# Optimization experiments

Hardware: AMD Instinct MI355X
Metric: run time of the kernel (lower is better)

Reference implementation:

```python
import jax, jax.numpy as jnp
import numpy as np

D = 300      # d_model / entity_embed_size, hard-coded in the module
TOPK = 20    # k in torch.topk


def setup_inputs() -> dict:
    key = jax.random.key(0)
    ks = jax.random.split(key, 6)
    N, T = 2, 4096
    scale = 1.0 / np.sqrt(D).astype(np.float32)
    return {
        "querys": jax.random.normal(ks[0], (N, T, D), jnp.float32),
        "keys":   jax.random.normal(ks[1], (N, T, D), jnp.float32),
        "values": jax.random.normal(ks[2], (N, T, D), jnp.float32),
        "Wq": jax.random.normal(ks[3], (D, D), jnp.float32) * scale,
        "Wk": jax.random.normal(ks[4], (D, D), jnp.float32) * scale,
        "Wv": jax.random.normal(ks[5], (D, D), jnp.float32) * scale,
        "num_heads": 6,
    }


def reference(querys, keys, values, Wq, Wk, Wv, num_heads):
    N, Tq, d = querys.shape
    h = int(num_heads)
    dh = d // h  # head dim (must divide; 300/6 = 50)

    # nn.Linear(bias=False): y = x @ W^T
    Q = querys @ Wq.T
    K = keys @ Wk.T
    V = values @ Wv.T  # computed but unused by the 'selected' attention, kept for fidelity

    # torch.cat(torch.split(X, dh, dim=2), dim=0): head index becomes major batch dim
    def to_heads(X):
        n, t, _ = X.shape
        return X.reshape(n, t, h, dh).transpose(2, 0, 1, 3).reshape(h * n, t, dh)

    Q_, K_ = to_heads(Q), to_heads(K)

    # scaled_dot_selected_product_attention
    scores = jnp.einsum('bqd,bkd->bqk', Q_, K_) / (dh ** 0.5)  # [hN, Tq, Tk]
    max_att = scores.max(axis=1)                                # [hN, Tk] (max over queries)
    top_vals, top_ids = jax.lax.top_k(max_att, TOPK)            # [hN, 20]
    probs = jax.nn.softmax(top_vals, axis=-1)                   # [hN, 20]
    # gather from K (not V!), matching the original code
    sel = jnp.take_along_axis(K_, top_ids[:, :, None], axis=1)  # [hN, 20, dh]
    out = jnp.sum(sel * probs[:, :, None], axis=1, keepdims=True)  # [hN, 1, dh]

    # torch.cat(torch.split(outputs, N, dim=0), dim=2): merge heads back on feature dim
    out = out.reshape(h, N, 1, dh).transpose(1, 2, 0, 3).reshape(N, 1, d)
    return out
```

## Files before the change

### kernel.cpp

```cpp
#include <hip/hip_runtime.h>
#include <hip/hip_bf16.h>
#include <math.h>

#define T      4096
#define Dm     300
#define NH     6
#define DH     50
#define NB     2
#define NBATCH 12
#define KTOP   20
#define NCAND  48
#define QC     4
#define RQC    16
#define NBINS  4096
#define BMAX   1024
#define WCH    30720
#define INITN  (NBATCH * T + NBATCH * NCAND + NBATCH)

typedef short  bs8  __attribute__((ext_vector_type(8)));
typedef float  f4   __attribute__((ext_vector_type(4)));

static __device__ __forceinline__ unsigned short f2bf(float f) {
    union { float f; unsigned u; } x{f};
    unsigned r = x.u + 0x7fffu + ((x.u >> 16) & 1u);
    return (unsigned short)(r >> 16);
}
static __device__ __forceinline__ float bf2f(unsigned short h) {
    union { unsigned u; float f; } x;
    x.u = ((unsigned)h) << 16;
    return x.f;
}
static __device__ __forceinline__ unsigned fkey(float f) {
    unsigned u = __float_as_uint(f);
    return (u & 0x80000000u) ? ~u : (u | 0x80000000u);
}
static __device__ __forceinline__ float fkey_inv(unsigned u) {
    return (u & 0x80000000u) ? __uint_as_float(u & 0x7fffffffu)
                             : __uint_as_float(~u);
}

__global__ __launch_bounds__(256) void wfrag_kernel(
    const float* __restrict__ Wq, const float* __restrict__ Wk,
    unsigned short* __restrict__ Whf, unsigned short* __restrict__ Wlf,
    unsigned* __restrict__ initp)
{
    for (unsigned g = blockIdx.x * 256 + threadIdx.x; g < INITN; g += gridDim.x * 256)
        initp[g] = 0u;

    const int idx = blockIdx.x * 256 + threadIdx.x;
    if (idx >= WCH) return;
    const int lane = idx & 63, rest = idx >> 6;
    const int ks = rest % 10, r2 = rest / 10;
    const int nt = r2 & 1, r3 = r2 >> 1;
    const int jtg = r3 % 12, z = r3 / 12;
    const int n16 = lane & 15, quad = lane >> 4;
    const int j = jtg * 32 + nt * 16 + n16;
    const int head = j >> 6, dd = j & 63;
    const float* W = z ? Wk : Wq;

    bs8 vh, vl;
#pragma unroll
    for (int e = 0; e < 8; ++e) {
        int k = ks * 32 + quad * 8 + e;
        float v = (dd < DH && k < 300) ? W[(head * DH + dd) * 300 + (k < 300 ? k : 0)] : 0.f;
        unsigned short h = f2bf(v);
        vh[e] = (short)h;
        vl[e] = (short)f2bf(v - bf2f(h));
    }
    *(bs8*)(Whf + (size_t)idx * 8) = vh;
    *(bs8*)(Wlf + (size_t)idx * 8) = vl;
}

__global__ __launch_bounds__(256, 1) void proj_mfma_kernel(
    const float* __restrict__ Xq, const float* __restrict__ Xk,
    const unsigned short* __restrict__ Whf, const unsigned short* __restrict__ Wlf,
    float* __restrict__ Qt, float* __restrict__ Kt,
    unsigned short* __restrict__ Qb, unsigned short* __restrict__ Kb)
{
    __shared__ unsigned short Bsh[2][2560 * 8];
    __shared__ unsigned short Tr[4][32][40];

    const int z  = blockIdx.z;
    const int jg = blockIdx.y;
    const int m0 = blockIdx.x * 128;
    const float* X = z ? Xk : Xq;
    float*          Ytf = z ? Kt : Qt;
    unsigned short* Ytb = z ? Kb : Qb;

    const int tid = threadIdx.x;
    const int wave = tid >> 6, lane = tid & 63;
    const int m16 = lane & 15, quad = lane >> 4;
    const int n = m0 >> 12, t0 = m0 & (T - 1);

    bs8 Ah[2][10], Al[2][10];
#pragma unroll
    for (int mt = 0; mt < 2; ++mt) {
        const float* rowp = X + (size_t)(m0 + wave * 32 + mt * 16 + m16) * 300;
#pragma unroll
        for (int ks = 0; ks < 10; ++ks) {
            float f[8];
            if (ks < 9) {
                float4 a = *(const float4*)(rowp + ks * 32 + quad * 8);
                float4 c = *(const float4*)(rowp + ks * 32 + quad * 8 + 4);
                f[0] = a.x; f[1] = a.y; f[2] = a.z; f[3] = a.w;
                f[4] = c.x; f[5] = c.y; f[6] = c.z; f[7] = c.w;
            } else {
#pragma unroll
                for (int e = 0; e < 8; ++e) {
                    int k = 288 + quad * 8 + e;
                    f[e] = (k < 300) ? rowp[k < 300 ? k : 0] : 0.f;
                }
            }
#pragma unroll
            for (int e = 0; e < 8; ++e) {
                unsigned short h = f2bf(f[e]);
                Ah[mt][ks][e] = (short)h;
                Al[mt][ks][e] = (short)f2bf(f[e] - bf2f(h));
            }
        }
    }

    bs8 rh[5], rl[5];
    {
        size_t cb = (size_t)(z * 12 + jg * 6) * 1280;
#pragma unroll
        for (int i = 0; i < 5; ++i) {
            int c = i * 256 + tid;
            rh[i] = *(const bs8*)(Whf + (cb + c) * 8);
            rl[i] = *(const bs8*)(Wlf + (cb + c) * 8);
        }
#pragma unroll
        for (int i = 0; i < 5; ++i) {
            int c = i * 256 + tid;
            *(bs8*)&Bsh[0][c * 8]          = rh[i];
            *(bs8*)&Bsh[0][(1280 + c) * 8] = rl[i];
        }
    }

    f4 acc[2][2] = {{{0.f,0.f,0.f,0.f},{0.f,0.f,0.f,0.f}},
                    {{0.f,0.f,0.f,0.f},{0.f,0.f,0.f,0.f}}};

    for (int jt = 0; jt < 6; ++jt) {
        __syncthreads();

        if (jt < 5) {
            size_t cb = (size_t)(z * 12 + jg * 6 + jt + 1) * 1280;
#pragma unroll
            for (int i = 0; i < 5; ++i) {
                int c = i * 256 + tid;
                rh[i] = *(const bs8*)(Whf + (cb + c) * 8);
                rl[i] = *(const bs8*)(Wlf + (cb + c) * 8);
            }
        }

        const unsigned short* Bbuf = Bsh[jt & 1];
#pragma unroll
        for (int ks = 0; ks < 10; ++ks) {
#pragma unroll
            for (int nt = 0; nt < 2; ++nt) {
                bs8 bh = *(const bs8*)&Bbuf[((nt * 10 + ks) * 64 + lane) * 8];
                bs8 bl = *(const bs8*)&Bbuf[((1280 + (nt * 10 + ks) * 64) + lane) * 8];
#pragma unroll
                for (int mt = 0; mt < 2; ++mt) {
                    acc[mt][nt] = __builtin_amdgcn_mfma_f32_16x16x32_bf16(Ah[mt][ks], bh, acc[mt][nt], 0, 0, 0);
                    acc[mt][nt] = __builtin_amdgcn_mfma_f32_16x16x32_bf16(Al[mt][ks], bh, acc[mt][nt], 0, 0, 0);
                    acc[mt][nt] = __builtin_amdgcn_mfma_f32_16x16x32_bf16(Ah[mt][ks], bl, acc[mt][nt], 0, 0, 0);
                }
            }
        }

        const int jtg  = jg * 6 + jt;
        const int head = jtg >> 1, d0 = (jtg & 1) * 32;
        const int b    = head * NB + n;

#pragma unroll
        for (int nt = 0; nt < 2; ++nt) {
            const int dd = d0 + nt * 16 + m16;
            if (dd < DH) {
                float* base = Ytf + ((size_t)b * DH + dd) * T + t0 + wave * 32;
#pragma unroll
                for (int mt = 0; mt < 2; ++mt)
                    *(float4*)(base + mt * 16 + quad * 4) =
                        make_float4(acc[mt][nt][0], acc[mt][nt][1], acc[mt][nt][2], acc[mt][nt][3]);
            }
        }

#pragma unroll
        for (int mt = 0; mt < 2; ++mt)
#pragma unroll
            for (int nt = 0; nt < 2; ++nt)
#pragma unroll
                for (int r = 0; r < 4; ++r)
                    Tr[wave][mt * 16 + quad * 4 + r][nt * 16 + m16] = f2bf(acc[mt][nt][r]);
        {
            const int rr = lane >> 1, p = lane & 1;
            unsigned short* dst = Ytb + ((size_t)b * T + t0 + wave * 32 + rr) * 64 + d0 + p * 16;
            *(bs8*)dst       = *(const bs8*)&Tr[wave][rr][p * 16];
            *(bs8*)(dst + 8) = *(const bs8*)&Tr[wave][rr][p * 16 + 8];
        }

#pragma unroll
        for (int mt = 0; mt < 2; ++mt)
#pragma unroll
            for (int nt = 0; nt < 2; ++nt)
                acc[mt][nt] = (f4){0.f, 0.f, 0.f, 0.f};

        __syncthreads();
        if (jt < 5) {
#pragma unroll
            for (int i = 0; i < 5; ++i) {
                int c = i * 256 + tid;
                *(bs8*)&Bsh[(jt + 1) & 1][c * 8]          = rh[i];
                *(bs8*)&Bsh[(jt + 1) & 1][(1280 + c) * 8] = rl[i];
            }
        }
    }
}

__global__ __launch_bounds__(256) void score_mfma_kernel(
    const unsigned short* __restrict__ Qb, const unsigned short* __restrict__ Kb,
    unsigned* __restrict__ pamax1)
{
    __shared__ unsigned short Qlds[2][1024 * 8];

    const int kb   = blockIdx.x;
    const int b    = blockIdx.y;
    const int qc   = blockIdx.z;
    const int tid  = threadIdx.x;
    const int wave = tid >> 6, lane = tid & 63;
    const int m16  = lane & 15, quad = lane >> 4;

    const int k0 = kb * 256 + wave * 64;

    bs8 Bf[4][2];
#pragma unroll
    for (int kt = 0; kt < 4; ++kt)
#pragma unroll
        for (int h = 0; h < 2; ++h)
            Bf[kt][h] = *(const bs8*)(Kb + ((size_t)(b * T + k0 + kt * 16 + m16)) * 64
                                         + quad * 8 + h * 32);

    float cmax[4];
#pragma unroll
    for (int kt = 0; kt < 4; ++kt) cmax[kt] = -INFINITY;

    const int r_ = tid >> 3, c2_ = tid & 7;
    bs8 pre[4];
#pragma unroll
    for (int i = 0; i < 4; ++i)
        pre[i] = *(const bs8*)(Qb + ((size_t)(b * T + qc * 1024 + i * 32 + r_)) * 64 + c2_ * 8);
#pragma unroll
    for (int i = 0; i < 4; ++i) {
        int row = i * 32 + r_;
        *(bs8*)&Qlds[0][(row * 8 + (c2_ ^ (row & 7))) * 8] = pre[i];
    }

    for (int it = 0; it < 8; ++it) {
        __syncthreads();
        if (it < 7) {
            const int q0 = qc * 1024 + (it + 1) * 128;
#pragma unroll
            for (int i = 0; i < 4; ++i)
                pre[i] = *(const bs8*)(Qb + ((size_t)(b * T + q0 + i * 32 + r_)) * 64 + c2_ * 8);
        }

        const unsigned short* Ql = Qlds[it & 1];
#pragma unroll
        for (int mt = 0; mt < 8; ++mt) {
            const int row = mt * 16 + m16;
            bs8 A0 = *(const bs8*)&Ql[(row * 8 + (quad ^ (row & 7))) * 8];
            bs8 A1 = *(const bs8*)&Ql[(row * 8 + ((quad + 4) ^ (row & 7))) * 8];
#pragma unroll
            for (int kt = 0; kt < 4; ++kt) {
                f4 acc = {0.f, 0.f, 0.f, 0.f};
                acc = __builtin_amdgcn_mfma_f32_16x16x32_bf16(A0, Bf[kt][0], acc, 0, 0, 0);
                acc = __builtin_amdgcn_mfma_f32_16x16x32_bf16(A1, Bf[kt][1], acc, 0, 0, 0);
                cmax[kt] = fmaxf(cmax[kt],
                                 fmaxf(fmaxf(acc[0], acc[1]), fmaxf(acc[2], acc[3])));
            }
        }
        __syncthreads();
        if (it < 7) {
#pragma unroll
            for (int i = 0; i < 4; ++i) {
                int row = i * 32 + r_;
                *(bs8*)&Qlds[(it + 1) & 1][(row * 8 + (c2_ ^ (row & 7))) * 8] = pre[i];
            }
        }
    }

#pragma unroll
    for (int kt = 0; kt < 4; ++kt) {
        float v = cmax[kt];
        v = fmaxf(v, __shfl_xor(v, 16));
        v = fmaxf(v, __shfl_xor(v, 32));
        if (lane < 16)
            atomicMax(&pamax1[(size_t)b * T + k0 + kt * 16 + lane], fkey(v));
    }
}

__global__ __launch_bounds__(256) void cand_kernel(
    const unsigned* __restrict__ pamax1, int* __restrict__ cand)
{
    __shared__ unsigned vals[T];
    __shared__ int      hist[NBINS];
    __shared__ int      part[256];
    __shared__ int      bidx[BMAX];
    __shared__ unsigned bval[BMAX];
    __shared__ int      candtmp[NCAND];
    __shared__ int      sh_B, sh_nout, sh_nb;

    const int b = blockIdx.x, tid = threadIdx.x;

    for (int i = tid; i < NBINS; i += 256) hist[i] = 0;
    if (tid == 0) { sh_nout = 0; sh_nb = 0; }
    __syncthreads();

    for (int i = tid; i < T; i += 256) {
        unsigned k = pamax1[(size_t)b * T + i];
        vals[i] = k;
        atomicAdd(&hist[k >> 20], 1);
    }
    __syncthreads();
    {
        int s = 0;
#pragma unroll
        for (int k = 0; k < 16; ++k) s += hist[tid * 16 + k];
        part[tid] = s;
        __syncthreads();
        for (int off = 1; off < 256; off <<= 1) {
            int v = (tid + off < 256) ? part[tid + off] : 0;
            __syncthreads();
            part[tid] += v;
            __syncthreads();
        }
        int run = (tid < 255) ? part[tid + 1] : 0;
        for (int k = 15; k >= 0; --k) {
            int bin = tid * 16 + k;
            int c = hist[bin];
            if (run < NCAND && run + c >= NCAND) sh_B = bin;
            run += c;
        }
    }
    __syncthreads();
    const int B = sh_B;

    for (int i = tid; i < T; i += 256) {
        int kb2 = (int)(vals[i] >> 20);
        if (kb2 > B) {
            int p = atomicAdd(&sh_nout, 1);
            candtmp[p] = i;
        } else if (kb2 == B) {
            int p = atomicAdd(&sh_nb, 1);
            if (p < BMAX) { bidx[p] = i; bval[p] = vals[i]; }
        }
    }
    __syncthreads();
    const int c1 = sh_nout, need = NCAND - c1;
    const int nb = (sh_nb < BMAX) ? sh_nb : BMAX;
    if (tid < 64) {
        for (int l = 0; l < need; ++l) {
            unsigned mv = 0; int mp = -1, mt = 0x7fffffff;
            for (int j = tid; j < nb; j += 64) {
                unsigned v = bval[j]; int t = bidx[j];
                if (v > mv || (v == mv && t < mt)) { mv = v; mp = j; mt = t; }
            }
#pragma unroll
            for (int off = 32; off > 0; off >>= 1) {
                unsigned v2 = (unsigned)__shfl_xor((int)mv, off);
                int p2 = __shfl_xor(mp, off);
                int t2 = __shfl_xor(mt, off);
                if (v2 > mv || (v2 == mv && t2 < mt)) { mv = v2; mp = p2; mt = t2; }
            }
            if (tid == 0) candtmp[c1 + l] = (mp >= 0) ? bidx[mp] : 0;
            if (mp >= 0 && tid == (mp & 63)) bval[mp] = 0;
        }
    }
    __syncthreads();

    if (tid < NCAND) {
        int myt = candtmp[tid], rank = 0;
        for (int j = 0; j < NCAND; ++j) rank += (candtmp[j] < myt);
        cand[b * NCAND + rank] = myt;
    }
}

__global__ __launch_bounds__(256) void rescore_final_kernel(
    const int* __restrict__ cand,
    const float* __restrict__ Qt, const float* __restrict__ Kt,
    unsigned* __restrict__ rmax1, unsigned* __restrict__ done_ct,
    float* __restrict__ out)
{
    __shared__ int   cand_s[NCAND];
    __shared__ float KcT[DH][NCAND];
    __shared__ float red[4][NCAND];
    __shared__ int   sh_pos;
    __shared__ float selval[KTOP];
    __shared__ int   selidx[KTOP];
    __shared__ float probs[KTOP];

    const int b = blockIdx.x, qch = blockIdx.y;
    const int tid = threadIdx.x, lane = tid & 63, wv = tid >> 6;

    if (tid < NCAND) cand_s[tid] = cand[b * NCAND + tid];
    __syncthreads();

    for (int i = tid; i < NCAND * DH; i += 256) {
        int j = i / DH, d = i - j * DH;
        KcT[d][j] = Kt[((size_t)b * DH + d) * T + cand_s[j]];
    }
    __syncthreads();

    const int q = qch * 256 + tid;
    float qv[DH];
#pragma unroll
    for (int d = 0; d < DH; ++d)
        qv[d] = Qt[((size_t)b * DH + d) * T + q];

    for (int g = 0; g < NCAND / 8; ++g) {
        float cm[8];
#pragma unroll
        for (int j = 0; j < 8; ++j) cm[j] = 0.f;
#pragma unroll
        for (int d = 0; d < DH; ++d) {
            float4 ka  = *(const float4*)&KcT[d][g * 8];
            float4 kb2 = *(const float4*)&KcT[d][g * 8 + 4];
            cm[0] = fmaf(qv[d], ka.x,  cm[0]);
            cm[1] = fmaf(qv[d], ka.y,  cm[1]);
            cm[2] = fmaf(qv[d], ka.z,  cm[2]);
            cm[3] = fmaf(qv[d], ka.w,  cm[3]);
            cm[4] = fmaf(qv[d], kb2.x, cm[4]);
            cm[5] = fmaf(qv[d], kb2.y, cm[5]);
            cm[6] = fmaf(qv[d], kb2.z, cm[6]);
            cm[7] = fmaf(qv[d], kb2.w, cm[7]);
        }
#pragma unroll
        for (int j = 0; j < 8; ++j) {
            float v = cm[j];
#pragma unroll
            for (int off = 32; off > 0; off >>= 1)
                v = fmaxf(v, __shfl_xor(v, off));
            if (lane == 0) red[wv][g * 8 + j] = v;
        }
    }
    __syncthreads();
    if (tid < NCAND) {
        float v = fmaxf(fmaxf(red[0][tid], red[1][tid]),
                        fmaxf(red[2][tid], red[3][tid]));
        atomicMax(&rmax1[b * NCAND + tid], fkey(v));
    }
    __syncthreads();
    if (tid == 0) {
        __threadfence();
        sh_pos = atomicAdd(&done_ct[b], 1u);
    }
    __syncthreads();
    if (sh_pos != RQC - 1) return;

    if (tid < 64) {
        float v = -INFINITY; int idx = 0x7fffffff;
        if (lane < NCAND) {
            unsigned u = atomicMax(&rmax1[b * NCAND + lane], 0u);
            v = fkey_inv(u) * 0.14142135623730951f;
            idx = cand_s[lane];
        }
        for (int l = 0; l < KTOP; ++l) {
            float mv = v; int mi = idx;
#pragma unroll
            for (int off = 32; off > 0; off >>= 1) {
                float v2 = __shfl_xor(mv, off);
                int   i2 = __shfl_xor(mi, off);
                if (v2 > mv || (v2 == mv && i2 < mi)) { mv = v2; mi = i2; }
            }
            if (idx == mi) v = -INFINITY;
            if (lane == 0) { selval[l] = mv; selidx[l] = mi; }
        }
    }
    __syncthreads();
    if (tid == 0) {
        float m = selval[0];
        float s = 0.f;
        for (int l = 0; l < KTOP; ++l) { float e = expf(selval[l] - m); probs[l] = e; s += e; }
        float inv = 1.f / s;
        for (int l = 0; l < KTOP; ++l) probs[l] *= inv;
    }
    __syncthreads();
    if (tid < DH) {
        float acc = 0.f;
#pragma unroll
        for (int l = 0; l < KTOP; ++l)
            acc += probs[l] * Kt[((size_t)b * DH + tid) * T + selidx[l]];
        int head = b / NB, n = b % NB;
        out[n * Dm + head * DH + tid] = acc;
    }
}

extern "C" void kernel_launch(void* const* d_in, const int* in_sizes, int n_in,
                              void* d_out, int out_size, void* d_ws, size_t ws_size,
                              hipStream_t stream) {
    const float* querys = (const float*)d_in[0];
    const float* keys   = (const float*)d_in[1];
    const float* Wq     = (const float*)d_in[3];
    const float* Wk     = (const float*)d_in[4];

    float* out = (float*)d_out;
    float* ws  = (float*)d_ws;

    float* Qt = ws;
    float* Kt = Qt + (size_t)NBATCH * DH * T;
    unsigned* pamax1  = (unsigned*)(Kt + (size_t)NBATCH * DH * T);
    unsigned* rmax1   = pamax1 + (size_t)NBATCH * T;
    unsigned* done_ct = rmax1 + (size_t)NBATCH * NCAND;
    int* cand = (int*)(done_ct + NBATCH);
    unsigned short* Qb = (unsigned short*)(cand + NBATCH * NCAND + 4);
    Qb = (unsigned short*)(((uintptr_t)Qb + 15) & ~(uintptr_t)15);
    unsigned short* Kb  = Qb  + (size_t)NBATCH * T * 64;
    unsigned short* Whf = Kb  + (size_t)NBATCH * T * 64;
    unsigned short* Wlf = Whf + (size_t)WCH * 8;

    wfrag_kernel      <<<(WCH + 255) / 256, 256, 0, stream>>>(Wq, Wk, Whf, Wlf, pamax1);
    proj_mfma_kernel  <<<dim3(64, 2, 2), 256, 0, stream>>>(querys, keys, Whf, Wlf, Qt, Kt, Qb, Kb);
    score_mfma_kernel <<<dim3(16, NBATCH, QC), 256, 0, stream>>>(Qb, Kb, pamax1);
    cand_kernel       <<<NBATCH, 256, 0, stream>>>(pamax1, cand);
    rescore_final_kernel<<<dim3(NBATCH, RQC), 256, 0, stream>>>(cand, Qt, Kt, rmax1, done_ct, out);
}
```

Measured before the change: 209.3 us.

## Pre-gather candidate K in cand kernel and split rescore by candidate across waves

The cand kernel now gathers the transposed K columns of the 48 candidates into a compact workspace buffer. The rescore kernel loads that buffer with contiguous float4 copies instead of doing a strided gather in every block. The rescore grid grows from 16 to 64 query chunks per batch. Each wave handles 64 queries against its own 12 candidates and issues atomicMax directly, with no shared-memory reduction. This spreads the small rescore tail over more blocks, at the cost of more global atomics and a serial gather inside the cand kernel.

```diff
diff --git a/kernel.cpp b/kernel.cpp
--- a/kernel.cpp
+++ b/kernel.cpp
@@ -11,7 +11,7 @@
 #define KTOP   20
 #define NCAND  48
 #define QC     4
-#define RQC    16
+#define RQC2   64
 #define NBINS  4096
 #define BMAX   1024
 #define WCH    30720
@@ -300,7 +300,8 @@
 }
 
 __global__ __launch_bounds__(256) void cand_kernel(
-    const unsigned* __restrict__ pamax1, int* __restrict__ cand)
+    const unsigned* __restrict__ pamax1, const float* __restrict__ Kt,
+    int* __restrict__ cand, float* __restrict__ candKT)
 {
     __shared__ unsigned vals[T];
     __shared__ int      hist[NBINS];
@@ -308,6 +309,7 @@
     __shared__ int      bidx[BMAX];
     __shared__ unsigned bval[BMAX];
     __shared__ int      candtmp[NCAND];
+    __shared__ int      cand_sorted[NCAND];
     __shared__ int      sh_B, sh_nout, sh_nb;
 
     const int b = blockIdx.x, tid = threadIdx.x;
@@ -381,19 +383,26 @@
     if (tid < NCAND) {
         int myt = candtmp[tid], rank = 0;
         for (int j = 0; j < NCAND; ++j) rank += (candtmp[j] < myt);
-        cand[b * NCAND + rank] = myt;
+        cand_sorted[rank] = myt;
+    }
+    __syncthreads();
+    if (tid < NCAND) cand[b * NCAND + tid] = cand_sorted[tid];
+
+    for (int i = tid; i < DH * NCAND; i += 256) {
+        int d = i / NCAND, j = i - d * NCAND;
+        candKT[(size_t)b * (DH * NCAND) + i] =
+            Kt[((size_t)b * DH + d) * T + cand_sorted[j]];
     }
 }
 
 __global__ __launch_bounds__(256) void rescore_final_kernel(
-    const int* __restrict__ cand,
+    const int* __restrict__ cand, const float* __restrict__ candKT,
     const float* __restrict__ Qt, const float* __restrict__ Kt,
     unsigned* __restrict__ rmax1, unsigned* __restrict__ done_ct,
     float* __restrict__ out)
 {
+    __shared__ float KcT[DH][NCAND];
     __shared__ int   cand_s[NCAND];
-    __shared__ float KcT[DH][NCAND];
-    __shared__ float red[4][NCAND];
     __shared__ int   sh_pos;
     __shared__ float selval[KTOP];
     __shared__ int   selidx[KTOP];
@@ -403,51 +412,47 @@
     const int tid = threadIdx.x, lane = tid & 63, wv = tid >> 6;
 
     if (tid < NCAND) cand_s[tid] = cand[b * NCAND + tid];
-    __syncthreads();
-
-    for (int i = tid; i < NCAND * DH; i += 256) {
-        int j = i / DH, d = i - j * DH;
-        KcT[d][j] = Kt[((size_t)b * DH + d) * T + cand_s[j]];
-    }
-    __syncthreads();
-
-    const int q = qch * 256 + tid;
+    for (int i = tid; i < DH * NCAND / 4; i += 256)
+        ((float4*)&KcT[0][0])[i] = ((const float4*)(candKT + (size_t)b * (DH * NCAND)))[i];
+    __syncthreads();
+
+    const int q = qch * 64 + lane;
     float qv[DH];
 #pragma unroll
     for (int d = 0; d < DH; ++d)
         qv[d] = Qt[((size_t)b * DH + d) * T + q];
 
-    for (int g = 0; g < NCAND / 8; ++g) {
-        float cm[8];
-#pragma unroll
-        for (int j = 0; j < 8; ++j) cm[j] = 0.f;
-#pragma unroll
-        for (int d = 0; d < DH; ++d) {
-            float4 ka  = *(const float4*)&KcT[d][g * 8];
-            float4 kb2 = *(const float4*)&KcT[d][g * 8 + 4];
-            cm[0] = fmaf(qv[d], ka.x,  cm[0]);
-            cm[1] = fmaf(qv[d], ka.y,  cm[1]);
-            cm[2] = fmaf(qv[d], ka.z,  cm[2]);
-            cm[3] = fmaf(qv[d], ka.w,  cm[3]);
-            cm[4] = fmaf(qv[d], kb2.x, cm[4]);
-            cm[5] = fmaf(qv[d], kb2.y, cm[5]);
-            cm[6] = fmaf(qv[d], kb2.z, cm[6]);
-            cm[7] = fmaf(qv[d], kb2.w, cm[7]);
-        }
-#pragma unroll
-        for (int j = 0; j < 8; ++j) {
-            float v = cm[j];
-#pragma unroll
-            for (int off = 32; off > 0; off >>= 1)
-                v = fmaxf(v, __shfl_xor(v, off));
-            if (lane == 0) red[wv][g * 8 + j] = v;
-        }
-    }
-    __syncthreads();
-    if (tid < NCAND) {
-        float v = fmaxf(fmaxf(red[0][tid], red[1][tid]),
-                        fmaxf(red[2][tid], red[3][tid]));
-        atomicMax(&rmax1[b * NCAND + tid], fkey(v));
+    const int j0 = wv * 12;
+    float cm[12];
+#pragma unroll
+    for (int j = 0; j < 12; ++j) cm[j] = 0.f;
+#pragma unroll
+    for (int d = 0; d < DH; ++d) {
+        float4 k0 = *(const float4*)&KcT[d][j0];
+        float4 k1 = *(const float4*)&KcT[d][j0 + 4];
+        float4 k2 = *(const float4*)&KcT[d][j0 + 8];
+        float x = qv[d];
+        cm[0]  = fmaf(x, k0.x, cm[0]);
+        cm[1]  = fmaf(x, k0.y, cm[1]);
+        cm[2]  = fmaf(x, k0.z, cm[2]);
+        cm[3]  = fmaf(x, k0.w, cm[3]);
+        cm[4]  = fmaf(x, k1.x, cm[4]);
+        cm[5]  = fmaf(x, k1.y, cm[5]);
+        cm[6]  = fmaf(x, k1.z, cm[6]);
+        cm[7]  = fmaf(x, k1.w, cm[7]);
+        cm[8]  = fmaf(x, k2.x, cm[8]);
+        cm[9]  = fmaf(x, k2.y, cm[9]);
+        cm[10] = fmaf(x, k2.z, cm[10]);
+        cm[11] = fmaf(x, k2.w, cm[11]);
+    }
+#pragma unroll
+    for (int j = 0; j < 12; ++j) {
+        float v = cm[j];
+#pragma unroll
+        for (int off = 32; off > 0; off >>= 1)
+            v = fmaxf(v, __shfl_xor(v, off));
+        if (lane == 0)
+            atomicMax(&rmax1[b * NCAND + j0 + j], fkey(v));
     }
     __syncthreads();
     if (tid == 0) {
@@ -455,7 +460,7 @@
         sh_pos = atomicAdd(&done_ct[b], 1u);
     }
     __syncthreads();
-    if (sh_pos != RQC - 1) return;
+    if (sh_pos != RQC2 - 1) return;
 
     if (tid < 64) {
         float v = -INFINITY; int idx = 0x7fffffff;
@@ -512,7 +517,8 @@
     unsigned* rmax1   = pamax1 + (size_t)NBATCH * T;
     unsigned* done_ct = rmax1 + (size_t)NBATCH * NCAND;
     int* cand = (int*)(done_ct + NBATCH);
-    unsigned short* Qb = (unsigned short*)(cand + NBATCH * NCAND + 4);
+    float* candKT = (float*)(cand + NBATCH * NCAND);
+    unsigned short* Qb = (unsigned short*)(candKT + (size_t)NBATCH * DH * NCAND + 4);
     Qb = (unsigned short*)(((uintptr_t)Qb + 15) & ~(uintptr_t)15);
     unsigned short* Kb  = Qb  + (size_t)NBATCH * T * 64;
     unsigned short* Whf = Kb  + (size_t)NBATCH * T * 64;
@@ -521,6 +527,6 @@
     wfrag_kernel      <<<(WCH + 255) / 256, 256, 0, stream>>>(Wq, Wk, Whf, Wlf, pamax1);
     proj_mfma_kernel  <<<dim3(64, 2, 2), 256, 0, stream>>>(querys, keys, Whf, Wlf, Qt, Kt, Qb, Kb);
     score_mfma_kernel <<<dim3(16, NBATCH, QC), 256, 0, stream>>>(Qb, Kb, pamax1);
-    cand_kernel       <<<NBATCH, 256, 0, stream>>>(pamax1, cand);
-    rescore_final_kernel<<<dim3(NBATCH, RQC), 256, 0, stream>>>(cand, Qt, Kt, rmax1, done_ct, out);
-}
+    cand_kernel       <<<NBATCH, 256, 0, stream>>>(pamax1, Kt, cand, candKT);
+    rescore_final_kernel<<<dim3(NBATCH, RQC2), 256, 0, stream>>>(cand, candKT, Qt, Kt, rmax1, done_ct, out);
+}
```

Result: slower. 264.7 us (+26.5%).
